# Kernel tuning notes

Hardware: AMD Instinct MI355X
Metric: run time of the kernel (lower is better)

Reference implementation:

```python
import jax, jax.numpy as jnp
import numpy as np

ROLLBACK = 1  # rollback_range: warp at 2**rollback finer resolution, then downsample
B, C, H, W = 2, 32, 512, 512
CIN = 3 * (C // 2) + 2  # inner module input channels


def _bilinear_warp(img, res):
    """Bilinear gather. img: [B,Cc,Hh,Ww]; res: [B,Hh,Ww,2] pixel offsets (x,y).
    Samples img at (x+res_x, y+res_y) with zero padding outside."""
    Bb, Cc, Hh, Ww = img.shape
    gy, gx = jnp.meshgrid(jnp.arange(Hh, dtype=img.dtype),
                          jnp.arange(Ww, dtype=img.dtype), indexing='ij')
    sx = gx[None] + res[..., 0]  # [B,Hh,Ww]
    sy = gy[None] + res[..., 1]
    x0 = jnp.floor(sx); y0 = jnp.floor(sy)
    wx = sx - x0; wy = sy - y0

    def gather(yi, xi):
        inb = ((yi >= 0) & (yi < Hh) & (xi >= 0) & (xi < Ww)).astype(img.dtype)
        yc = jnp.clip(yi, 0, Hh - 1).astype(jnp.int32)
        xc = jnp.clip(xi, 0, Ww - 1).astype(jnp.int32)
        v = jax.vmap(lambda im, y, x: im[:, y, x])(img, yc, xc)  # [B,Cc,Hh,Ww]
        return v * inb[:, None]

    v00 = gather(y0, x0);     v01 = gather(y0, x0 + 1)
    v10 = gather(y0 + 1, x0); v11 = gather(y0 + 1, x0 + 1)
    wx = wx[:, None]; wy = wy[:, None]  # broadcast over channels
    return (v00 * (1 - wy) * (1 - wx) + v01 * (1 - wy) * wx
            + v10 * wy * (1 - wx) + v11 * wy * wx)


def _resize_img(img, f):  # [B,Cc,Hh,Ww] bilinear spatial resize
    Bb, Cc, Hh, Ww = img.shape
    return jax.image.resize(img, (Bb, Cc, int(Hh * f), int(Ww * f)), 'bilinear')


def _resize_res(res, f):  # [B,Hh,Ww,2]; pixel-unit values scale with resolution
    Bb, Hh, Ww, _ = res.shape
    return jax.image.resize(res, (Bb, int(Hh * f), int(Ww * f), 2), 'bilinear') * f


def res_warp_img(img, res, rollback):
    if rollback > 0:
        f = 2 ** rollback
        out = _bilinear_warp(_resize_img(img, f), _resize_res(res, f))
        return _resize_img(out, 1.0 / f)
    return _bilinear_warp(img, res)


def res_warp_res(res_a, res_b, rollback):
    # warp residual field a (treated as a 2-channel image, values in pixel units) by b
    if rollback > 0:
        f = 2 ** rollback
        a = _resize_res(res_a, f); b = _resize_res(res_b, f)
        out = jnp.transpose(_bilinear_warp(jnp.transpose(a, (0, 3, 1, 2)), b), (0, 2, 3, 1))
        return _resize_res(out, 1.0 / f)
    out = _bilinear_warp(jnp.transpose(res_a, (0, 3, 1, 2)), res_b)
    return jnp.transpose(out, (0, 2, 3, 1))


def combine_residuals(res_a, res_b, rollback):
    # flow composition: apply a then b
    return res_b + res_warp_res(res_a, res_b, rollback)


def _conv3x3(x, w, b):
    y = jax.lax.conv_general_dilated(x, w, (1, 1), 'SAME',
                                     dimension_numbers=('NCHW', 'OIHW', 'NCHW'))
    return y + b[None, :, None, None]


def setup_inputs() -> dict:
    key = jax.random.key(0)
    k1, k2, k3 = jax.random.split(key, 3)
    x = jax.random.normal(k1, (B, C, H, W), dtype=jnp.float32)
    res = jax.random.normal(k2, (B, 2, H, W), dtype=jnp.float32)  # ~1px flow
    W_inner = jax.random.normal(k3, (2, CIN, 3, 3), dtype=jnp.float32) * 0.02
    b_inner = jnp.zeros((2,), dtype=jnp.float32)
    return {"x": x, "res": res, "W_inner": W_inner, "b_inner": b_inner, "level": 0}


def reference(x, res, W_inner, b_inner, level):
    res_hw = jnp.transpose(res, (0, 2, 3, 1))  # [B,H,W,2]
    nf = x.shape[1]
    src, tgt = x[:, :nf // 2], x[:, nf // 2:]
    warped_tgt = res_warp_img(tgt, res_hw, ROLLBACK)
    bundle = jnp.concatenate([src, tgt, warped_tgt, res], axis=1)  # [B,3C/2+2,H,W]
    adj = _conv3x3(bundle, W_inner, b_inner)  # hindsight_adjustment [B,2,H,W]
    # mode == 'combine_res': state['down'][level]['input'] = combined residual
    new_res = combine_residuals(res_hw, jnp.transpose(adj, (0, 2, 3, 1)), ROLLBACK)
    hindsight_warped_tgt = res_warp_img(tgt, new_res, ROLLBACK)
    return jnp.concatenate([src, hindsight_warped_tgt], axis=1)  # [B,C,H,W]
```

## Files before the change

### kernel.cpp

```cpp
#include <hip/hip_runtime.h>
#include <hip/hip_bf16.h>
#include <cstdint>
#include <cstddef>

#define HW   512
#define HW2  1024
#define SZ   (512 * 512)
#define NPT  (34 * 34)
#define K_PTS 5
#define SRCW 36
#define NSRC (SRCW * SRCW)
#define MARG 9
#define FDIM 18
#define NFLD (FDIM * FDIM)

struct UpTap { int i0, i1; float w0, w1; };

__device__ __forceinline__ UpTap up_tap(int i) {
  UpTap t;
  int k = i >> 1;
  if ((i & 1) == 0) {
    t.i0 = k - 1; t.i1 = k; t.w0 = 0.25f; t.w1 = 0.75f;
    if (k == 0) { t.i0 = 0; t.w0 = 0.0f; t.w1 = 1.0f; }
  } else {
    t.i0 = k; t.i1 = k + 1; t.w0 = 0.75f; t.w1 = 0.25f;
    if (k == HW - 1) { t.i1 = HW - 1; t.w0 = 1.0f; t.w1 = 0.0f; }
  }
  return t;
}

__device__ __forceinline__ float2 up_at2(const float2* __restrict__ f,
                                         int yi, int xi, int oy, int ox) {
  UpTap ty = up_tap(yi), tx = up_tap(xi);
  const float2* r0 = f + (ty.i0 - oy) * FDIM - ox;
  const float2* r1 = f + (ty.i1 - oy) * FDIM - ox;
  float2 v00 = r0[tx.i0], v01 = r0[tx.i1];
  float2 v10 = r1[tx.i0], v11 = r1[tx.i1];
  float2 r;
  r.x = ty.w0 * (tx.w0 * v00.x + tx.w1 * v01.x) + ty.w1 * (tx.w0 * v10.x + tx.w1 * v11.x);
  r.y = ty.w0 * (tx.w0 * v00.y + tx.w1 * v01.y) + ty.w1 * (tx.w0 * v10.y + tx.w1 * v11.y);
  return r;
}

__device__ __forceinline__ void axis_taps(float s, int& base, float& w0, float& w1, float& w2) {
  float f0 = floorf(s);
  int i0 = (int)f0;
  float fr = s - f0;
  int b = (i0 & 1) ? (i0 >> 1) : (i0 >> 1) - 1;
  b = b < 0 ? 0 : (b > (HW - 3) ? (HW - 3) : b);
  float w[3] = {0.0f, 0.0f, 0.0f};
  if ((unsigned)i0 < (unsigned)HW2) {
    UpTap t = up_tap(i0);
    w[t.i0 - b] += (1.0f - fr) * t.w0;
    w[t.i1 - b] += (1.0f - fr) * t.w1;
  }
  if ((unsigned)(i0 + 1) < (unsigned)HW2) {
    UpTap t = up_tap(i0 + 1);
    w[t.i0 - b] += fr * t.w0;
    w[t.i1 - b] += fr * t.w1;
  }
  base = b; w0 = w[0]; w1 = w[1]; w2 = w[2];
}

struct PtTaps {
  int   locoff;
  float wy0, wy1, wy2, wx0, wx1, wx2;
};

__device__ __forceinline__ void stage_field(const float* __restrict__ fx,
                                            const float* __restrict__ fy,
                                            float2* __restrict__ sf,
                                            int fy0, int fx0, int tid) {
  #pragma unroll
  for (int i = 0; i < 2; ++i) {
    int p = tid + i * 256;
    if (p < NFLD) {
      int r = p / FDIM, c = p % FDIM;
      int gy = fy0 + r; gy = gy < 0 ? 0 : (gy > HW - 1 ? HW - 1 : gy);
      int gx = fx0 + c; gx = gx < 0 ? 0 : (gx > HW - 1 ? HW - 1 : gx);
      size_t o = (size_t)gy * HW + gx;
      sf[p] = make_float2(fx[o], fy[o]);
    }
  }
}

__device__ __forceinline__ void compute_taps(const float2* __restrict__ sf,
                                             int fy0, int fx0,
                                             int gx0, int gy0, int xo, int yo, int tid,
                                             PtTaps (&pt)[K_PTS]) {
  #pragma unroll
  for (int i = 0; i < K_PTS; ++i) {
    int p = tid + i * 256;
    pt[i].locoff = 0;
    pt[i].wy0 = pt[i].wy1 = pt[i].wy2 = 0.0f;
    pt[i].wx0 = pt[i].wx1 = pt[i].wx2 = 0.0f;
    if (p < NPT) {
      int ry = p / 34, rx = p % 34;
      int yy = gy0 + ry, xx = gx0 + rx;
      if ((unsigned)yy < (unsigned)HW2 && (unsigned)xx < (unsigned)HW2) {
        float2 d = up_at2(sf, yy, xx, fy0, fx0);
        float sx = (float)xx + 2.0f * d.x;
        float sy = (float)yy + 2.0f * d.y;
        int bx, by;
        axis_taps(sx, bx, pt[i].wx0, pt[i].wx1, pt[i].wx2);
        axis_taps(sy, by, pt[i].wy0, pt[i].wy1, pt[i].wy2);
        int rx_ = bx - xo, ry_ = by - yo;
        if ((unsigned)rx_ <= (unsigned)(SRCW - 3) && (unsigned)ry_ <= (unsigned)(SRCW - 3))
          pt[i].locoff = ry_ * SRCW + rx_;
        else
          pt[i].locoff = ~(by * HW + bx);
      }
    }
  }
}

__device__ __forceinline__ void stage_pair(const float* __restrict__ p0,
                                           const float* __restrict__ p1,
                                           float2* __restrict__ s_src,
                                           int xo, int yo, int tid) {
  #pragma unroll
  for (int i = 0; i < 6; ++i) {
    int p = tid + i * 256;
    if (p < NSRC) {
      int r = p / SRCW, c = p % SRCW;
      int gy = yo + r; gy = gy < 0 ? 0 : (gy > HW - 1 ? HW - 1 : gy);
      int gx = xo + c; gx = gx < 0 ? 0 : (gx > HW - 1 ? HW - 1 : gx);
      size_t o = (size_t)gy * HW + gx;
      s_src[p] = make_float2(p0[o], p1[o]);
    }
  }
}

__device__ __forceinline__ float eval3_global(const float* __restrict__ pl, int off, const PtTaps& t) {
  const float* p0 = pl + off;
  float r0 = t.wx0 * p0[0]        + t.wx1 * p0[1]          + t.wx2 * p0[2];
  float r1 = t.wx0 * p0[HW]       + t.wx1 * p0[HW + 1]     + t.wx2 * p0[HW + 2];
  float r2 = t.wx0 * p0[2 * HW]   + t.wx1 * p0[2 * HW + 1] + t.wx2 * p0[2 * HW + 2];
  return t.wy0 * r0 + t.wy1 * r1 + t.wy2 * r2;
}

__device__ __forceinline__ void eval_round(const float2* __restrict__ s_src,
                                           float2* __restrict__ s_tile,
                                           const float* __restrict__ plane0,
                                           const float* __restrict__ plane1,
                                           const PtTaps (&pt)[K_PTS], int tid) {
  #pragma unroll
  for (int i = 0; i < K_PTS; ++i) {
    int p = tid + i * 256;
    if (p < NPT) {
      const PtTaps t = pt[i];
      float a0, a1;
      if (t.locoff >= 0) {
        const float2* s = s_src + t.locoff;
        float2 v00 = s[0],        v01 = s[1],            v02 = s[2];
        float2 v10 = s[SRCW],     v11 = s[SRCW + 1],     v12 = s[SRCW + 2];
        float2 v20 = s[2 * SRCW], v21 = s[2 * SRCW + 1], v22 = s[2 * SRCW + 2];
        float r00 = t.wx0 * v00.x + t.wx1 * v01.x + t.wx2 * v02.x;
        float r10 = t.wx0 * v10.x + t.wx1 * v11.x + t.wx2 * v12.x;
        float r20 = t.wx0 * v20.x + t.wx1 * v21.x + t.wx2 * v22.x;
        float r01 = t.wx0 * v00.y + t.wx1 * v01.y + t.wx2 * v02.y;
        float r11 = t.wx0 * v10.y + t.wx1 * v11.y + t.wx2 * v12.y;
        float r21 = t.wx0 * v20.y + t.wx1 * v21.y + t.wx2 * v22.y;
        a0 = t.wy0 * r00 + t.wy1 * r10 + t.wy2 * r20;
        a1 = t.wy0 * r01 + t.wy1 * r11 + t.wy2 * r21;
      } else {
        int off = ~t.locoff;
        a0 = eval3_global(plane0, off, t);
        a1 = eval3_global(plane1, off, t);
      }
      s_tile[p] = make_float2(a0, a1);
    }
  }
}

__global__ void warp_img_kernel(const float* __restrict__ x,
                                const float* __restrict__ res,
                                float* __restrict__ out)
{
  __shared__ float2 s_src[NSRC];
  __shared__ float2 s_tile[NPT];

  const int b = blockIdx.z;
  const int tx0 = blockIdx.x * 16, ty0 = blockIdx.y * 16;
  const int gx0 = tx0 * 2 - 1, gy0 = ty0 * 2 - 1;
  const int xo = tx0 - MARG, yo = ty0 - MARG;
  const int fy0 = ty0 - 1, fx0 = tx0 - 1;
  const int tid = threadIdx.x;

  const float* resx = res + (size_t)b * 2 * SZ;
  const float* resy = resx + SZ;
  const float* tgt  = x + ((size_t)b * 32 + 16) * SZ;

  stage_pair(tgt, tgt + SZ, s_src, xo, yo, tid);
  stage_field(resx, resy, s_tile, fy0, fx0, tid);

  const int ly = tid >> 4, lx = tid & 15;
  const int oy = ty0 + ly, ox = tx0 + lx;
  const float RW[4] = {0.25f, 0.75f, 0.75f, 0.25f};
  float wy[4], wx[4];
  float sumy = 0.f, sumx = 0.f;
  #pragma unroll
  for (int d = 0; d < 4; ++d) {
    int g = 2 * oy - 1 + d;
    wy[d] = ((unsigned)g < (unsigned)HW2) ? RW[d] : 0.0f; sumy += wy[d];
    g = 2 * ox - 1 + d;
    wx[d] = ((unsigned)g < (unsigned)HW2) ? RW[d] : 0.0f; sumx += wx[d];
  }
  const float inv = 1.0f / (sumy * sumx);

  __syncthreads();

  PtTaps pt[K_PTS];
  compute_taps(s_tile, fy0, fx0, gx0, gy0, xo, yo, tid, pt);

  __syncthreads();

  for (int c = 0; c < 16; c += 2) {
    const float* plane0 = tgt + (size_t)c * SZ;
    eval_round(s_src, s_tile, plane0, plane0 + SZ, pt, tid);
    __syncthreads();

    if (c < 14)
      stage_pair(plane0 + 2 * SZ, plane0 + 3 * SZ, s_src, xo, yo, tid);

    float acc0 = 0.0f, acc1 = 0.0f;
    #pragma unroll
    for (int dy = 0; dy < 4; ++dy) {
      float r0 = 0.0f, r1 = 0.0f;
      const int base = (2 * ly + dy) * 34 + 2 * lx;
      #pragma unroll
      for (int dx = 0; dx < 4; ++dx) {
        float2 v = s_tile[base + dx];
        r0 += wx[dx] * v.x;
        r1 += wx[dx] * v.y;
      }
      acc0 += wy[dy] * r0;
      acc1 += wy[dy] * r1;
    }
    size_t o = (((size_t)b * 32 + 16 + c) * HW + oy) * HW + ox;
    out[o] = acc0 * inv;
    out[o + SZ] = acc1 * inv;
    __syncthreads();
  }
}

#define CHN 18
#define CHE (CHN * CHN)

__global__ void __launch_bounds__(256)
conv_kernel(const float* __restrict__ x,
            const float* __restrict__ res,
            const float* __restrict__ Wc,
            const float* __restrict__ bc,
            float* __restrict__ out,
            float* __restrict__ adj)
{
  __shared__ float sh[8][CHE];

  const int tid = threadIdx.x;
  const int b = blockIdx.z;
  const int tx0 = blockIdx.x * 16, ty0 = blockIdx.y * 16;
  const int ty = tid >> 4, tx = tid & 15;

  const float* px = x + (size_t)b * 32 * SZ;
  const float* pw = out + ((size_t)b * 32 + 16) * SZ;
  const float* pr = res + (size_t)b * 2 * SZ;

  const int ry0 = tid / CHN, rx0 = tid - ry0 * CHN;
  const int hy0 = ty0 - 1 + ry0, hx0 = tx0 - 1 + rx0;
  const bool ok0 = (unsigned)hy0 < (unsigned)HW && (unsigned)hx0 < (unsigned)HW;
  const int off0 = hy0 * HW + hx0;
  const int p1 = tid + 256;
  const bool sl1 = p1 < CHE;
  const int ry1 = p1 / CHN, rx1 = p1 - ry1 * CHN;
  const int hy1 = ty0 - 1 + ry1, hx1 = tx0 - 1 + rx1;
  const bool ok1 = sl1 && (unsigned)hy1 < (unsigned)HW && (unsigned)hx1 < (unsigned)HW;
  const int off1 = hy1 * HW + hx1;

  #define PLANE(ic) ((ic) < 32 ? px + (size_t)(ic) * SZ \
                   : (ic) < 48 ? pw + (size_t)((ic) - 32) * SZ \
                   : pr + (size_t)((ic) - 48) * SZ)

  float acc0 = bc[0];
  float acc1 = bc[1];

  float q0[4], q1[4];
  {
    #pragma unroll
    for (int j = 0; j < 4; ++j) {
      const float* pl = PLANE(j);
      q0[j] = ok0 ? pl[off0] : 0.f;
      q1[j] = ok1 ? pl[off1] : 0.f;
    }
    #pragma unroll
    for (int j = 0; j < 4; ++j) {
      sh[j][tid] = q0[j];
      if (sl1) sh[j][p1] = q1[j];
    }
  }

  const size_t pix = (size_t)(ty0 + ty) * HW + (tx0 + tx);

  for (int kk = 0; kk < 12; ++kk) {
    __syncthreads();
    if (kk < 11) {
      #pragma unroll
      for (int j = 0; j < 4; ++j) {
        const float* pl = PLANE(4 * kk + 4 + j);
        q0[j] = ok0 ? pl[off0] : 0.f;
        q1[j] = ok1 ? pl[off1] : 0.f;
      }
    } else {
      #pragma unroll
      for (int j = 0; j < 2; ++j) {
        const float* pl = PLANE(48 + j);
        q0[j] = ok0 ? pl[off0] : 0.f;
        q1[j] = ok1 ? pl[off1] : 0.f;
      }
    }

    const int cur = (kk & 1) * 4;
    const float* w0 = Wc + (size_t)(4 * kk) * 9;
    const float* w1 = Wc + 450 + (size_t)(4 * kk) * 9;
    float cen[4];
    #pragma unroll
    for (int ky = 0; ky < 3; ++ky) {
      #pragma unroll
      for (int kx = 0; kx < 3; ++kx) {
        const int hoff = (ty + ky) * CHN + tx + kx;
        const int widx = ky * 3 + kx;
        #pragma unroll
        for (int j = 0; j < 4; ++j) {
          float v = sh[cur + j][hoff];
          if (ky == 1 && kx == 1) cen[j] = v;
          acc0 += v * w0[j * 9 + widx];
          acc1 += v * w1[j * 9 + widx];
        }
      }
    }

    if (kk < 4) {
      #pragma unroll
      for (int j = 0; j < 4; ++j)
        out[((size_t)b * 32 + 4 * kk + j) * SZ + pix] = cen[j];
    }

    const int nxt = cur ^ 4;
    if (kk < 11) {
      #pragma unroll
      for (int j = 0; j < 4; ++j) {
        sh[nxt + j][tid] = q0[j];
        if (sl1) sh[nxt + j][p1] = q1[j];
      }
    } else {
      #pragma unroll
      for (int j = 0; j < 2; ++j) {
        sh[nxt + j][tid] = q0[j];
        if (sl1) sh[nxt + j][p1] = q1[j];
      }
    }
  }

  __syncthreads();
  {
    const float* w0 = Wc + (size_t)48 * 9;
    const float* w1 = Wc + 450 + (size_t)48 * 9;
    #pragma unroll
    for (int ky = 0; ky < 3; ++ky) {
      #pragma unroll
      for (int kx = 0; kx < 3; ++kx) {
        const int hoff = (ty + ky) * CHN + tx + kx;
        const int widx = ky * 3 + kx;
        #pragma unroll
        for (int j = 0; j < 2; ++j) {
          float v = sh[j][hoff];
          acc0 += v * w0[j * 9 + widx];
          acc1 += v * w1[j * 9 + widx];
        }
      }
    }
  }
  #undef PLANE

  adj[((size_t)b * 2 + 0) * SZ + pix] = acc0;
  adj[((size_t)b * 2 + 1) * SZ + pix] = acc1;
}

__global__ void new_res_kernel(const float* __restrict__ res,
                               const float* __restrict__ adj,
                               float* __restrict__ nres)
{
  __shared__ float2 s_src[NSRC];
  __shared__ float2 s_tile[NPT];

  const int b = blockIdx.z;
  const int tx0 = blockIdx.x * 16, ty0 = blockIdx.y * 16;
  const int gx0 = tx0 * 2 - 1, gy0 = ty0 * 2 - 1;
  const int xo = tx0 - MARG, yo = ty0 - MARG;
  const int fy0 = ty0 - 1, fx0 = tx0 - 1;
  const int tid = threadIdx.x;

  const float* adjx = adj + (size_t)b * 2 * SZ;
  const float* adjy = adjx + SZ;
  const float* res0 = res + (size_t)b * 2 * SZ;
  const float* res1 = res0 + SZ;

  stage_pair(res0, res1, s_src, xo, yo, tid);
  stage_field(adjx, adjy, s_tile, fy0, fx0, tid);

  const int ly = tid >> 4, lx = tid & 15;
  const int oy = ty0 + ly, ox = tx0 + lx;
  const float RW[4] = {0.25f, 0.75f, 0.75f, 0.25f};
  float wy[4], wx[4];
  float sumy = 0.f, sumx = 0.f;
  #pragma unroll
  for (int d = 0; d < 4; ++d) {
    int g = 2 * oy - 1 + d;
    wy[d] = ((unsigned)g < (unsigned)HW2) ? RW[d] : 0.0f; sumy += wy[d];
    g = 2 * ox - 1 + d;
    wx[d] = ((unsigned)g < (unsigned)HW2) ? RW[d] : 0.0f; sumx += wx[d];
  }
  const float inv = 1.0f / (sumy * sumx);

  __syncthreads();

  PtTaps pt[K_PTS];
  compute_taps(s_tile, fy0, fx0, gx0, gy0, xo, yo, tid, pt);

  __syncthreads();

  eval_round(s_src, s_tile, res0, res1, pt, tid);
  __syncthreads();

  float acc0 = 0.0f, acc1 = 0.0f;
  #pragma unroll
  for (int dy = 0; dy < 4; ++dy) {
    float r0 = 0.0f, r1 = 0.0f;
    const int base = (2 * ly + dy) * 34 + 2 * lx;
    #pragma unroll
    for (int dx = 0; dx < 4; ++dx) {
      float2 v = s_tile[base + dx];
      r0 += wx[dx] * v.x;
      r1 += wx[dx] * v.y;
    }
    acc0 += wy[dy] * r0;
    acc1 += wy[dy] * r1;
  }
  size_t o = ((size_t)b * 2) * SZ + (size_t)oy * HW + ox;
  nres[o]      = acc0 * inv + adjx[(size_t)oy * HW + ox];
  nres[o + SZ] = acc1 * inv + adjy[(size_t)oy * HW + ox];
}

extern "C" void kernel_launch(void* const* d_in, const int* in_sizes, int n_in,
                              void* d_out, int out_size, void* d_ws, size_t ws_size,
                              hipStream_t stream) {
  const float* x   = (const float*)d_in[0];
  const float* res = (const float*)d_in[1];
  const float* Wc  = (const float*)d_in[2];
  const float* bc  = (const float*)d_in[3];
  float* out = (float*)d_out;

  float* adj  = (float*)d_ws;
  float* nres = adj + (size_t)2 * 2 * SZ;

  dim3 tile_grid(32, 32, 2);

  warp_img_kernel<<<tile_grid, dim3(256), 0, stream>>>(x, res, out);

  conv_kernel<<<tile_grid, dim3(256), 0, stream>>>(x, res, Wc, bc, out, adj);

  new_res_kernel<<<tile_grid, dim3(256), 0, stream>>>(res, adj, nres);

  warp_img_kernel<<<tile_grid, dim3(256), 0, stream>>>(x, nres, out);
}
```

Baseline: 372.6 us.

## Fuse new-residual computation into final hindsight warp kernel

```diff
diff --git a/kernel.cpp b/kernel.cpp
--- a/kernel.cpp
+++ b/kernel.cpp
@@ -13,6 +13,11 @@
 #define MARG 9
 #define FDIM 18
 #define NFLD (FDIM * FDIM)
+#define SRCW2 38
+#define NSRC2 (SRCW2 * SRCW2)
+#define MARG2 10
+#define ADIM 20
+#define NADJ (ADIM * ADIM)
 
 struct UpTap { int i0, i1; float w0, w1; };
 
@@ -29,11 +34,11 @@
   return t;
 }
 
-__device__ __forceinline__ float2 up_at2(const float2* __restrict__ f,
-                                         int yi, int xi, int oy, int ox) {
+__device__ __forceinline__ float2 up_at2s(const float2* __restrict__ f,
+                                          int yi, int xi, int oy, int ox, int stride) {
   UpTap ty = up_tap(yi), tx = up_tap(xi);
-  const float2* r0 = f + (ty.i0 - oy) * FDIM - ox;
-  const float2* r1 = f + (ty.i1 - oy) * FDIM - ox;
+  const float2* r0 = f + (ty.i0 - oy) * stride - ox;
+  const float2* r1 = f + (ty.i1 - oy) * stride - ox;
   float2 v00 = r0[tx.i0], v01 = r0[tx.i1];
   float2 v10 = r1[tx.i0], v11 = r1[tx.i1];
   float2 r;
@@ -98,7 +103,7 @@
       int ry = p / 34, rx = p % 34;
       int yy = gy0 + ry, xx = gx0 + rx;
       if ((unsigned)yy < (unsigned)HW2 && (unsigned)xx < (unsigned)HW2) {
-        float2 d = up_at2(sf, yy, xx, fy0, fx0);
+        float2 d = up_at2s(sf, yy, xx, fy0, fx0, FDIM);
         float sx = (float)xx + 2.0f * d.x;
         float sy = (float)yy + 2.0f * d.y;
         int bx, by;
@@ -386,27 +391,52 @@
   adj[((size_t)b * 2 + 1) * SZ + pix] = acc1;
 }
 
-__global__ void new_res_kernel(const float* __restrict__ res,
-                               const float* __restrict__ adj,
-                               float* __restrict__ nres)
+__global__ void hindsight_kernel(const float* __restrict__ x,
+                                 const float* __restrict__ res,
+                                 const float* __restrict__ adj,
+                                 float* __restrict__ out)
 {
-  __shared__ float2 s_src[NSRC];
-  __shared__ float2 s_tile[NPT];
+  __shared__ float2 sA[NSRC2];
+  __shared__ float2 sB[NSRC2];
+  __shared__ float2 sC[NADJ];
+  __shared__ float2 sF[NFLD];
 
   const int b = blockIdx.z;
   const int tx0 = blockIdx.x * 16, ty0 = blockIdx.y * 16;
   const int gx0 = tx0 * 2 - 1, gy0 = ty0 * 2 - 1;
   const int xo = tx0 - MARG, yo = ty0 - MARG;
   const int fy0 = ty0 - 1, fx0 = tx0 - 1;
+  const int yo2 = ty0 - MARG2, xo2 = tx0 - MARG2;
   const int tid = threadIdx.x;
 
   const float* adjx = adj + (size_t)b * 2 * SZ;
   const float* adjy = adjx + SZ;
   const float* res0 = res + (size_t)b * 2 * SZ;
   const float* res1 = res0 + SZ;
-
-  stage_pair(res0, res1, s_src, xo, yo, tid);
-  stage_field(adjx, adjy, s_tile, fy0, fx0, tid);
+  const float* tgt  = x + ((size_t)b * 32 + 16) * SZ;
+
+  #pragma unroll
+  for (int i = 0; i < 6; ++i) {
+    int p = tid + i * 256;
+    if (p < NSRC2) {
+      int r = p / SRCW2, c = p % SRCW2;
+      int gy = yo2 + r; gy = gy < 0 ? 0 : (gy > HW - 1 ? HW - 1 : gy);
+      int gx = xo2 + c; gx = gx < 0 ? 0 : (gx > HW - 1 ? HW - 1 : gx);
+      size_t o = (size_t)gy * HW + gx;
+      sB[p] = make_float2(res0[o], res1[o]);
+    }
+  }
+  #pragma unroll
+  for (int i = 0; i < 2; ++i) {
+    int p = tid + i * 256;
+    if (p < NADJ) {
+      int r = p / ADIM, c = p % ADIM;
+      int gy = ty0 - 2 + r; gy = gy < 0 ? 0 : (gy > HW - 1 ? HW - 1 : gy);
+      int gx = tx0 - 2 + c; gx = gx < 0 ? 0 : (gx > HW - 1 ? HW - 1 : gx);
+      size_t o = (size_t)gy * HW + gx;
+      sC[p] = make_float2(adjx[o], adjy[o]);
+    }
+  }
 
   const int ly = tid >> 4, lx = tid & 15;
   const int oy = ty0 + ly, ox = tx0 + lx;
@@ -424,31 +454,120 @@
 
   __syncthreads();
 
+  {
+    const int qy0 = 2 * fy0 - 1, qx0 = 2 * fx0 - 1;
+    #pragma unroll
+    for (int i = 0; i < 6; ++i) {
+      int p = tid + i * 256;
+      if (p < NSRC2) {
+        int r = p / SRCW2, c = p % SRCW2;
+        int qy = qy0 + r, qx = qx0 + c;
+        float a0 = 0.f, a1 = 0.f;
+        if ((unsigned)qy < (unsigned)HW2 && (unsigned)qx < (unsigned)HW2) {
+          float2 d = up_at2s(sC, qy, qx, ty0 - 2, tx0 - 2, ADIM);
+          float sxx = (float)qx + 2.0f * d.x;
+          float syy = (float)qy + 2.0f * d.y;
+          PtTaps t;
+          int bx, by;
+          axis_taps(sxx, bx, t.wx0, t.wx1, t.wx2);
+          axis_taps(syy, by, t.wy0, t.wy1, t.wy2);
+          int rx_ = bx - xo2, ry_ = by - yo2;
+          if ((unsigned)rx_ <= (unsigned)(SRCW2 - 3) && (unsigned)ry_ <= (unsigned)(SRCW2 - 3)) {
+            const float2* s = sB + ry_ * SRCW2 + rx_;
+            float2 v00 = s[0],         v01 = s[1],             v02 = s[2];
+            float2 v10 = s[SRCW2],     v11 = s[SRCW2 + 1],     v12 = s[SRCW2 + 2];
+            float2 v20 = s[2 * SRCW2], v21 = s[2 * SRCW2 + 1], v22 = s[2 * SRCW2 + 2];
+            float r00 = t.wx0 * v00.x + t.wx1 * v01.x + t.wx2 * v02.x;
+            float r10 = t.wx0 * v10.x + t.wx1 * v11.x + t.wx2 * v12.x;
+            float r20 = t.wx0 * v20.x + t.wx1 * v21.x + t.wx2 * v22.x;
+            float r01 = t.wx0 * v00.y + t.wx1 * v01.y + t.wx2 * v02.y;
+            float r11 = t.wx0 * v10.y + t.wx1 * v11.y + t.wx2 * v12.y;
+            float r21 = t.wx0 * v20.y + t.wx1 * v21.y + t.wx2 * v22.y;
+            a0 = t.wy0 * r00 + t.wy1 * r10 + t.wy2 * r20;
+            a1 = t.wy0 * r01 + t.wy1 * r11 + t.wy2 * r21;
+          } else {
+            int off = by * HW + bx;
+            a0 = eval3_global(res0, off, t);
+            a1 = eval3_global(res1, off, t);
+          }
+        }
+        sA[p] = make_float2(a0, a1);
+      }
+    }
+  }
+  __syncthreads();
+
+  #pragma unroll
+  for (int i = 0; i < 2; ++i) {
+    int p = tid + i * 256;
+    if (p < NFLD) {
+      int pr = p / FDIM, pc = p % FDIM;
+      int py = fy0 + pr; py = py < 0 ? 0 : (py > HW - 1 ? HW - 1 : py);
+      int px = fx0 + pc; px = px < 0 ? 0 : (px > HW - 1 ? HW - 1 : px);
+      float wyv[4], wxv[4];
+      float sy = 0.f, sx = 0.f;
+      #pragma unroll
+      for (int d = 0; d < 4; ++d) {
+        int g = 2 * py - 1 + d;
+        wyv[d] = ((unsigned)g < (unsigned)HW2) ? RW[d] : 0.0f; sy += wyv[d];
+        g = 2 * px - 1 + d;
+        wxv[d] = ((unsigned)g < (unsigned)HW2) ? RW[d] : 0.0f; sx += wxv[d];
+      }
+      float inv2 = 1.0f / (sy * sx);
+      float a0 = 0.f, a1 = 0.f;
+      #pragma unroll
+      for (int dy = 0; dy < 4; ++dy) {
+        float r0 = 0.f, r1 = 0.f;
+        const int base = (2 * (py - fy0) + dy) * SRCW2 + 2 * (px - fx0);
+        #pragma unroll
+        for (int dx = 0; dx < 4; ++dx) {
+          float2 v = sA[base + dx];
+          r0 += wxv[dx] * v.x;
+          r1 += wxv[dx] * v.y;
+        }
+        a0 += wyv[dy] * r0;
+        a1 += wyv[dy] * r1;
+      }
+      float2 ac = sC[(py - (ty0 - 2)) * ADIM + (px - (tx0 - 2))];
+      sF[p] = make_float2(a0 * inv2 + ac.x, a1 * inv2 + ac.y);
+    }
+  }
+  __syncthreads();
+
+  stage_pair(tgt, tgt + SZ, sA, xo, yo, tid);
+
   PtTaps pt[K_PTS];
-  compute_taps(s_tile, fy0, fx0, gx0, gy0, xo, yo, tid, pt);
-
-  __syncthreads();
-
-  eval_round(s_src, s_tile, res0, res1, pt, tid);
-  __syncthreads();
-
-  float acc0 = 0.0f, acc1 = 0.0f;
-  #pragma unroll
-  for (int dy = 0; dy < 4; ++dy) {
-    float r0 = 0.0f, r1 = 0.0f;
-    const int base = (2 * ly + dy) * 34 + 2 * lx;
-    #pragma unroll
-    for (int dx = 0; dx < 4; ++dx) {
-      float2 v = s_tile[base + dx];
-      r0 += wx[dx] * v.x;
-      r1 += wx[dx] * v.y;
-    }
-    acc0 += wy[dy] * r0;
-    acc1 += wy[dy] * r1;
-  }
-  size_t o = ((size_t)b * 2) * SZ + (size_t)oy * HW + ox;
-  nres[o]      = acc0 * inv + adjx[(size_t)oy * HW + ox];
-  nres[o + SZ] = acc1 * inv + adjy[(size_t)oy * HW + ox];
+  compute_taps(sF, fy0, fx0, gx0, gy0, xo, yo, tid, pt);
+
+  __syncthreads();
+
+  for (int c = 0; c < 16; c += 2) {
+    const float* plane0 = tgt + (size_t)c * SZ;
+    eval_round(sA, sB, plane0, plane0 + SZ, pt, tid);
+    __syncthreads();
+
+    if (c < 14)
+      stage_pair(plane0 + 2 * SZ, plane0 + 3 * SZ, sA, xo, yo, tid);
+
+    float acc0 = 0.0f, acc1 = 0.0f;
+    #pragma unroll
+    for (int dy = 0; dy < 4; ++dy) {
+      float r0 = 0.0f, r1 = 0.0f;
+      const int base = (2 * ly + dy) * 34 + 2 * lx;
+      #pragma unroll
+      for (int dx = 0; dx < 4; ++dx) {
+        float2 v = sB[base + dx];
+        r0 += wx[dx] * v.x;
+        r1 += wx[dx] * v.y;
+      }
+      acc0 += wy[dy] * r0;
+      acc1 += wy[dy] * r1;
+    }
+    size_t o = (((size_t)b * 32 + 16 + c) * HW + oy) * HW + ox;
+    out[o] = acc0 * inv;
+    out[o + SZ] = acc1 * inv;
+    __syncthreads();
+  }
 }
 
 extern "C" void kernel_launch(void* const* d_in, const int* in_sizes, int n_in,
@@ -460,8 +579,7 @@
   const float* bc  = (const float*)d_in[3];
   float* out = (float*)d_out;
 
-  float* adj  = (float*)d_ws;
-  float* nres = adj + (size_t)2 * 2 * SZ;
+  float* adj = (float*)d_ws;
 
   dim3 tile_grid(32, 32, 2);
 
@@ -469,7 +587,5 @@
 
   conv_kernel<<<tile_grid, dim3(256), 0, stream>>>(x, res, Wc, bc, out, adj);
 
-  new_res_kernel<<<tile_grid, dim3(256), 0, stream>>>(res, adj, nres);
-
-  warp_img_kernel<<<tile_grid, dim3(256), 0, stream>>>(x, nres, out);
-}
+  hindsight_kernel<<<tile_grid, dim3(256), 0, stream>>>(x, res, adj, out);
+}
```

Result: no change. 370.1 us (-0.7%).
